# Kernel optimization log

Hardware: AMD Instinct MI355X
Metric: run time of the kernel (lower is better)

Reference implementation:

```python
import jax, jax.numpy as jnp
import numpy as np

B, T = 2, 2048
V, C, H = 32000, 1024, 16
HS = C // H  # 64
W_SCALE = 0.02


def setup_inputs() -> dict:
    key = jax.random.key(0)
    ks = jax.random.split(key, 8)
    x = jax.random.randint(ks[0], (B, T), 0, V)
    tok_emb = jax.random.normal(ks[1], (V, C), jnp.float32) * W_SCALE
    pos_emb = jax.random.normal(ks[2], (T, C), jnp.float32) * W_SCALE
    wq = jax.random.normal(ks[3], (H, C, HS), jnp.float32) * W_SCALE
    wk = jax.random.normal(ks[4], (H, C, HS), jnp.float32) * W_SCALE
    wv = jax.random.normal(ks[5], (H, C, HS), jnp.float32) * W_SCALE
    bq = jnp.zeros((H, HS), jnp.float32)
    bk = jnp.zeros((H, HS), jnp.float32)
    bv = jnp.zeros((H, HS), jnp.float32)
    w_head = jax.random.normal(ks[6], (C, V), jnp.float32) * W_SCALE
    b_head = jnp.zeros((V,), jnp.float32)
    return dict(x=x, tok_emb=tok_emb, pos_emb=pos_emb, wq=wq, bq=bq,
                wk=wk, bk=bk, wv=wv, bv=bv, w_head=w_head, b_head=b_head)


def reference(x, tok_emb, pos_emb, wq, bq, wk, bk, wv, bv, w_head, b_head):
    Bx, Tx = x.shape
    Cx = tok_emb.shape[1]
    h = tok_emb[x] + pos_emb[:Tx]  # [B,T,C]
    # all heads batched: per-head Linear layers stacked on leading H axis
    q = jnp.einsum('btc,hcd->bhtd', h, wq) + bq[None, :, None, :]
    k = jnp.einsum('btc,hcd->bhtd', h, wk) + bk[None, :, None, :]
    v = jnp.einsum('btc,hcd->bhtd', h, wv) + bv[None, :, None, :]
    # NOTE: original scales by n_embd**-0.5 (full C), not head_size**-0.5
    att = jnp.einsum('bhtd,bhsd->bhts', q, k) * (Cx ** -0.5)
    causal = jnp.tril(jnp.ones((Tx, Tx), dtype=bool))
    att = jnp.where(causal, att, jnp.finfo(att.dtype).min)
    att = jax.nn.softmax(att, axis=-1)
    y = jnp.einsum('bhts,bhsd->bhtd', att, v)  # [B,H,T,HS]
    y = jnp.transpose(y, (0, 2, 1, 3)).reshape(Bx, Tx, Cx)  # concat heads
    logits = jnp.einsum('btc,cv->btv', y, w_head) + b_head  # [B,T,V]
    return logits
```

## Files before the change

kernel.cpp:

```cpp
#include <hip/hip_runtime.h>

#define T_SEQ 2048
#define C_DIM 1024
#define H_N   16
#define HS_D  64
#define V_DIM 32000

typedef float f32x4 __attribute__((ext_vector_type(4)));
typedef __bf16 bf16x8 __attribute__((ext_vector_type(8)));
typedef unsigned short us4 __attribute__((ext_vector_type(4)));
typedef unsigned short us8 __attribute__((ext_vector_type(8)));

__device__ inline unsigned short f2bf(float f) {
  unsigned int u = __float_as_uint(f);
  u = (u + 0x7FFFu + ((u >> 16) & 1u)) >> 16;
  return (unsigned short)u;
}

__global__ __launch_bounds__(256) void embed_kernel(
    const int* __restrict__ x, const float* __restrict__ tok,
    const float* __restrict__ pos, unsigned short* __restrict__ h) {
  int idx = blockIdx.x * 256 + threadIdx.x;
  int bt = idx >> 8;
  int c4 = (idx & 255) * 4;
  int t = bt & (T_SEQ - 1);
  int tokid = x[bt];
  f32x4 a = *(const f32x4*)(tok + (size_t)tokid * C_DIM + c4);
  f32x4 b = *(const f32x4*)(pos + (size_t)t * C_DIM + c4);
  f32x4 s = a + b;
  us4 o;
  o[0] = f2bf(s[0]); o[1] = f2bf(s[1]); o[2] = f2bf(s[2]); o[3] = f2bf(s[3]);
  *(us4*)(h + (size_t)bt * C_DIM + c4) = o;
}

__global__ __launch_bounds__(256) void repack_qkv(
    const float* __restrict__ wq, const float* __restrict__ wk, const float* __restrict__ wv,
    const float* __restrict__ bq, const float* __restrict__ bk, const float* __restrict__ bv,
    unsigned short* __restrict__ wt, float* __restrict__ biasp) {
  int which = blockIdx.y;
  const float* w = (which == 0) ? wq : (which == 1) ? wk : wv;
  int i = blockIdx.x * 256 + threadIdx.x;
  int d = i & 63;
  int c = (i >> 6) & (C_DIM - 1);
  int hh = i >> 16;
  int n = which * 1024 + hh * 64 + d;
  wt[(size_t)n * C_DIM + c] = f2bf(w[i]);
  if (c == 0) {
    const float* bb = (which == 0) ? bq : (which == 1) ? bk : bv;
    biasp[n] = bb[hh * 64 + d];
  }
}

__global__ __launch_bounds__(256) void repack_whead(
    const float* __restrict__ wh, unsigned short* __restrict__ wht) {
  __shared__ float tile[64][65];
  int v0 = blockIdx.x * 64;
  int c0 = blockIdx.y * 64;
  int tr = threadIdx.x >> 6;
  int tc = threadIdx.x & 63;
#pragma unroll
  for (int i = 0; i < 16; ++i) {
    int r = i * 4 + tr;
    tile[r][tc] = wh[(size_t)(c0 + r) * V_DIM + v0 + tc];
  }
  __syncthreads();
#pragma unroll
  for (int i = 0; i < 16; ++i) {
    int vr = i * 4 + tr;
    wht[(size_t)(v0 + vr) * C_DIM + c0 + tc] = f2bf(tile[tc][vr]);
  }
}

#define GK 1024
#define GBK 32
#define GNT 32

__global__ __launch_bounds__(512, 2) void gemm256(
    const unsigned short* __restrict__ A, const unsigned short* __restrict__ Bt,
    const float* __restrict__ bias, float* __restrict__ Cout, int N, int Mtiles) {
  __shared__ unsigned short As[4][256 * 32];
  __shared__ unsigned short Bs[4][256 * 32];
  int tid = threadIdx.x;
  int lane = tid & 63;
  int wid = tid >> 6;
  int wm = wid >> 2, wn = wid & 3;
  int l16 = lane & 15, g = lane >> 4;
  int swz = (l16 & 3) ^ ((l16 >> 2) & 3);

  int cpx = gridDim.x >> 3;
  int lin = blockIdx.x;
  int wg = (lin & 7) * cpx + (lin >> 3);
  int m0 = (wg % Mtiles) * 256;
  int n0 = (wg / Mtiles) * 256;

  auto stage = [&](const unsigned short* __restrict__ G, int t0,
                   unsigned short* lds, int kt) {
#pragma unroll
    for (int L = 0; L < 2; ++L) {
      int chunk = L * 512 + tid;
      int row = chunk >> 2;
      int c = (chunk & 3) ^ (row & 3) ^ ((row >> 2) & 3);
      const unsigned short* ga = G + (size_t)(t0 + row) * GK + kt * GBK + c * 8;
      __builtin_amdgcn_global_load_lds(
          (const __attribute__((address_space(1))) void*)ga,
          (__attribute__((address_space(3))) void*)(lds + chunk * 8), 16, 0, 0);
    }
  };

#pragma unroll
  for (int kt = 0; kt < 3; ++kt) {
    stage(A, m0, As[kt], kt);
    stage(Bt, n0, Bs[kt], kt);
  }

  f32x4 acc[8][4] = {};

  for (int t = 0; t < GNT; ++t) {
    int buf = t & 3;
    if (t + 2 < GNT)      asm volatile("s_waitcnt vmcnt(8)" ::: "memory");
    else if (t + 1 < GNT) asm volatile("s_waitcnt vmcnt(4)" ::: "memory");
    else                  asm volatile("s_waitcnt vmcnt(0)" ::: "memory");
    asm volatile("s_barrier" ::: "memory");

    const char* Ab = (const char*)As[buf];
    const char* Bb = (const char*)Bs[buf];

    bf16x8 bfr[4], af[4];
#pragma unroll
    for (int n = 0; n < 4; ++n) {
      int row = wn * 64 + n * 16 + l16;
      bfr[n] = *(const bf16x8*)(Bb + row * 64 + ((g ^ swz) * 16));
    }
#pragma unroll
    for (int m = 0; m < 4; ++m) {
      int row = wm * 128 + m * 16 + l16;
      af[m] = *(const bf16x8*)(Ab + row * 64 + ((g ^ swz) * 16));
    }
    if (t + 3 < GNT) stage(A, m0, As[(t + 3) & 3], t + 3);
    __builtin_amdgcn_s_setprio(1);
#pragma unroll
    for (int m = 0; m < 4; ++m)
#pragma unroll
      for (int n = 0; n < 4; ++n)
        acc[m][n] = __builtin_amdgcn_mfma_f32_16x16x32_bf16(af[m], bfr[n], acc[m][n], 0, 0, 0);
    __builtin_amdgcn_s_setprio(0);
    asm volatile("s_barrier" ::: "memory");

#pragma unroll
    for (int m = 0; m < 4; ++m) {
      int row = wm * 128 + 64 + m * 16 + l16;
      af[m] = *(const bf16x8*)(Ab + row * 64 + ((g ^ swz) * 16));
    }
    if (t + 3 < GNT) stage(Bt, n0, Bs[(t + 3) & 3], t + 3);
    __builtin_amdgcn_s_setprio(1);
#pragma unroll
    for (int m = 0; m < 4; ++m)
#pragma unroll
      for (int n = 0; n < 4; ++n)
        acc[4 + m][n] = __builtin_amdgcn_mfma_f32_16x16x32_bf16(af[m], bfr[n], acc[4 + m][n], 0, 0, 0);
    __builtin_amdgcn_s_setprio(0);
  }

#pragma unroll
  for (int m = 0; m < 8; ++m) {
    int mh = m >> 2, mi = m & 3;
    int row = m0 + wm * 128 + mh * 64 + mi * 16 + g * 4;
#pragma unroll
    for (int n = 0; n < 4; ++n) {
      int col = n0 + wn * 64 + n * 16 + l16;
      float bv = bias[col];
#pragma unroll
      for (int j = 0; j < 4; ++j)
        Cout[(size_t)(row + j) * N + col] = acc[m][n][j] + bv;
    }
  }
}

__global__ __launch_bounds__(256) void attn_mfma(
    const float* __restrict__ qkv, unsigned short* __restrict__ y) {
  __shared__ char lds[24576];
  char* Kl = lds;
  char* Vl = lds + 8192;
  char* Pl = lds + 16384;

  int bh = blockIdx.y;
  int b = bh >> 4, h = bh & 15;
  int qb = (T_SEQ / 64 - 1) - blockIdx.x;
  int tid = threadIdx.x;
  int lane = tid & 63, w = tid >> 6;
  int l16 = lane & 15, g = lane >> 4;
  size_t bT = (size_t)b * T_SEQ;
  const float scale = 0.03125f;

  bf16x8 qf[2];
  {
    const float* qrow = qkv + (bT + qb * 64 + w * 16 + l16) * 3072 + h * 64;
#pragma unroll
    for (int kk = 0; kk < 2; ++kk) {
      f32x4 a = *(const f32x4*)(qrow + kk * 32 + g * 8);
      f32x4 c = *(const f32x4*)(qrow + kk * 32 + g * 8 + 4);
      us8 o;
      o[0] = f2bf(a[0]); o[1] = f2bf(a[1]); o[2] = f2bf(a[2]); o[3] = f2bf(a[3]);
      o[4] = f2bf(c[0]); o[5] = f2bf(c[1]); o[6] = f2bf(c[2]); o[7] = f2bf(c[3]);
      qf[kk] = *(bf16x8*)&o;
    }
  }

  f32x4 yacc[4] = {};
  float mrun[4], lrun[4];
#pragma unroll
  for (int j = 0; j < 4; ++j) { mrun[j] = -3.0e38f; lrun[j] = 0.f; }

  int srow = tid >> 2;
  int c0 = (tid & 3) * 16;

  for (int kb = 0; kb <= qb; ++kb) {
    {
      const float* kp = qkv + (bT + kb * 64 + srow) * 3072 + 1024 + h * 64 + c0;
      f32x4 k0 = *(const f32x4*)(kp + 0);
      f32x4 k1 = *(const f32x4*)(kp + 4);
      f32x4 k2 = *(const f32x4*)(kp + 8);
      f32x4 k3 = *(const f32x4*)(kp + 12);
      us8 pa, pb;
      pa[0]=f2bf(k0[0]); pa[1]=f2bf(k0[1]); pa[2]=f2bf(k0[2]); pa[3]=f2bf(k0[3]);
      pa[4]=f2bf(k1[0]); pa[5]=f2bf(k1[1]); pa[6]=f2bf(k1[2]); pa[7]=f2bf(k1[3]);
      pb[0]=f2bf(k2[0]); pb[1]=f2bf(k2[1]); pb[2]=f2bf(k2[2]); pb[3]=f2bf(k2[3]);
      pb[4]=f2bf(k3[0]); pb[5]=f2bf(k3[1]); pb[6]=f2bf(k3[2]); pb[7]=f2bf(k3[3]);
      *(us8*)(Kl + ((srow * 128 + c0 * 2)      ^ ((srow & 7) << 4))) = pa;
      *(us8*)(Kl + ((srow * 128 + c0 * 2 + 16) ^ ((srow & 7) << 4))) = pb;
      const float* vp = kp + 1024;
      f32x4 v0 = *(const f32x4*)(vp + 0);
      f32x4 v1 = *(const f32x4*)(vp + 4);
      f32x4 v2 = *(const f32x4*)(vp + 8);
      f32x4 v3 = *(const f32x4*)(vp + 12);
      float vals[16] = {v0[0],v0[1],v0[2],v0[3], v1[0],v1[1],v1[2],v1[3],
                        v2[0],v2[1],v2[2],v2[3], v3[0],v3[1],v3[2],v3[3]};
#pragma unroll
      for (int i = 0; i < 16; ++i) {
        int ch = c0 + i;
        *(unsigned short*)(Vl + ((ch * 128 + srow * 2) ^ ((ch & 7) << 4))) = f2bf(vals[i]);
      }
    }
    __syncthreads();

    f32x4 s[4] = {};
#pragma unroll
    for (int kk = 0; kk < 2; ++kk)
#pragma unroll
      for (int n = 0; n < 4; ++n) {
        int krow = n * 16 + l16;
        bf16x8 fb = *(const bf16x8*)(Kl + ((krow * 128 + (kk * 32 + g * 8) * 2) ^ ((krow & 7) << 4)));
        s[n] = __builtin_amdgcn_mfma_f32_16x16x32_bf16(qf[kk], fb, s[n], 0, 0, 0);
      }

    bool diag = (kb == qb);
    float pr[4][4];
    float corr[4];
#pragma unroll
    for (int j = 0; j < 4; ++j) {
      int rloc = w * 16 + g * 4 + j;
      float m = -3.0e38f;
#pragma unroll
      for (int n = 0; n < 4; ++n) {
        float v = s[n][j] * scale;
        if (diag && (n * 16 + l16) > rloc) v = -3.0e38f;
        pr[n][j] = v;
        m = fmaxf(m, v);
      }
      m = fmaxf(m, __shfl_xor(m, 1));
      m = fmaxf(m, __shfl_xor(m, 2));
      m = fmaxf(m, __shfl_xor(m, 4));
      m = fmaxf(m, __shfl_xor(m, 8));
      float mn = fmaxf(mrun[j], m);
      corr[j] = __expf(mrun[j] - mn);
      mrun[j] = mn;
      float ps = 0.f;
#pragma unroll
      for (int n = 0; n < 4; ++n) {
        float e = __expf(pr[n][j] - mn);
        pr[n][j] = e;
        ps += e;
      }
      ps += __shfl_xor(ps, 1);
      ps += __shfl_xor(ps, 2);
      ps += __shfl_xor(ps, 4);
      ps += __shfl_xor(ps, 8);
      lrun[j] = lrun[j] * corr[j] + ps;
    }
#pragma unroll
    for (int n = 0; n < 4; ++n)
#pragma unroll
      for (int j = 0; j < 4; ++j)
        yacc[n][j] *= corr[j];

#pragma unroll
    for (int j = 0; j < 4; ++j) {
      int row = w * 16 + g * 4 + j;
#pragma unroll
      for (int n = 0; n < 4; ++n)
        *(unsigned short*)(Pl + ((row * 128 + (n * 16 + l16) * 2) ^ ((row & 7) << 4))) = f2bf(pr[n][j]);
    }

#pragma unroll
    for (int kk = 0; kk < 2; ++kk) {
      int prow = w * 16 + l16;
      bf16x8 fa = *(const bf16x8*)(Pl + ((prow * 128 + (kk * 32 + g * 8) * 2) ^ ((prow & 7) << 4)));
#pragma unroll
      for (int n = 0; n < 4; ++n) {
        int vrow = n * 16 + l16;
        bf16x8 fb = *(const bf16x8*)(Vl + ((vrow * 128 + (kk * 32 + g * 8) * 2) ^ ((vrow & 7) << 4)));
        yacc[n] = __builtin_amdgcn_mfma_f32_16x16x32_bf16(fa, fb, yacc[n], 0, 0, 0);
      }
    }
    __syncthreads();
  }

#pragma unroll
  for (int j = 0; j < 4; ++j) {
    float inv = 1.0f / lrun[j];
    int row = qb * 64 + w * 16 + g * 4 + j;
    unsigned short* yo = y + (bT + row) * C_DIM + h * 64;
#pragma unroll
    for (int n = 0; n < 4; ++n)
      yo[n * 16 + l16] = f2bf(yacc[n][j] * inv);
  }
}

extern "C" void kernel_launch(void* const* d_in, const int* in_sizes, int n_in,
                              void* d_out, int out_size, void* d_ws, size_t ws_size,
                              hipStream_t stream) {
  const int*   x    = (const int*)d_in[0];
  const float* tok  = (const float*)d_in[1];
  const float* pos  = (const float*)d_in[2];
  const float* wq   = (const float*)d_in[3];
  const float* bq   = (const float*)d_in[4];
  const float* wk   = (const float*)d_in[5];
  const float* bk   = (const float*)d_in[6];
  const float* wv   = (const float*)d_in[7];
  const float* bv   = (const float*)d_in[8];
  const float* wh   = (const float*)d_in[9];
  const float* bhd  = (const float*)d_in[10];
  float* out = (float*)d_out;

  char* ws = (char*)d_ws;
  size_t off = 0;
  auto alloc = [&](size_t bytes) {
    void* p = ws + off;
    off += (bytes + 255) & ~(size_t)255;
    return p;
  };
  unsigned short* h_bf    = (unsigned short*)alloc((size_t)4096 * 1024 * 2);
  unsigned short* wqkv_t  = (unsigned short*)alloc((size_t)3072 * 1024 * 2);
  float*          qbias   = (float*)alloc((size_t)3072 * 4);
  unsigned short* wh_t    = (unsigned short*)alloc((size_t)V_DIM * 1024 * 2);
  float*          qkv     = (float*)alloc((size_t)4096 * 3072 * 4);
  unsigned short* ybf     = (unsigned short*)alloc((size_t)4096 * 1024 * 2);

  embed_kernel<<<4096, 256, 0, stream>>>(x, tok, pos, h_bf);
  repack_qkv<<<dim3(4096, 3), 256, 0, stream>>>(wq, wk, wv, bq, bk, bv, wqkv_t, qbias);
  repack_whead<<<dim3(V_DIM / 64, 16), 256, 0, stream>>>(wh, wh_t);
  gemm256<<<192, 512, 0, stream>>>(h_bf, wqkv_t, qbias, qkv, 3072, 16);
  attn_mfma<<<dim3(T_SEQ / 64, 2 * H_N), 256, 0, stream>>>(qkv, ybf);
  gemm256<<<2000, 512, 0, stream>>>(ybf, wh_t, bhd, out, V_DIM, 16);
}
```

Baseline: 664.9 us.

## Restructure GEMM to single-buffer BK=64 with per-quarter streaming of A tiles

The GEMM drops the 4-deep ring of 32-wide K tiles and uses one 256x64 LDS buffer each for A and B, with an 8-way XOR swizzle. The next A tile is refilled in four row-quarters, each issued right after the matching quarter has been read into registers, while MFMAs on the current data run. B is staged once per K step. This frees LDS so more blocks can be resident and halves the number of K iterations, but adds more barriers and leaves less prefetch depth to hide global latency.

```diff
diff --git a/kernel.cpp b/kernel.cpp
--- a/kernel.cpp
+++ b/kernel.cpp
@@ -72,20 +72,18 @@
 }
 
 #define GK 1024
-#define GBK 32
-#define GNT 32
+#define GNT 16
 
 __global__ __launch_bounds__(512, 2) void gemm256(
     const unsigned short* __restrict__ A, const unsigned short* __restrict__ Bt,
     const float* __restrict__ bias, float* __restrict__ Cout, int N, int Mtiles) {
-  __shared__ unsigned short As[4][256 * 32];
-  __shared__ unsigned short Bs[4][256 * 32];
+  __shared__ unsigned short As[256 * 64];
+  __shared__ unsigned short Bs[256 * 64];
   int tid = threadIdx.x;
   int lane = tid & 63;
   int wid = tid >> 6;
   int wm = wid >> 2, wn = wid & 3;
   int l16 = lane & 15, g = lane >> 4;
-  int swz = (l16 & 3) ^ ((l16 >> 2) & 3);
 
   int cpx = gridDim.x >> 3;
   int lin = blockIdx.x;
@@ -93,85 +91,93 @@
   int m0 = (wg % Mtiles) * 256;
   int n0 = (wg / Mtiles) * 256;
 
-  auto stage = [&](const unsigned short* __restrict__ G, int t0,
-                   unsigned short* lds, int kt) {
-#pragma unroll
-    for (int L = 0; L < 2; ++L) {
-      int chunk = L * 512 + tid;
-      int row = chunk >> 2;
-      int c = (chunk & 3) ^ (row & 3) ^ ((row >> 2) & 3);
-      const unsigned short* ga = G + (size_t)(t0 + row) * GK + kt * GBK + c * 8;
+  auto stageB = [&](int kt) {
+#pragma unroll
+    for (int q = 0; q < 4; ++q) {
+      int chunk = q * 512 + tid;
+      int row = chunk >> 3, cpos = chunk & 7;
+      int c = cpos ^ (row & 7);
+      const unsigned short* src = Bt + (size_t)(n0 + row) * GK + kt * 64 + c * 8;
       __builtin_amdgcn_global_load_lds(
-          (const __attribute__((address_space(1))) void*)ga,
-          (__attribute__((address_space(3))) void*)(lds + chunk * 8), 16, 0, 0);
+          (const __attribute__((address_space(1))) void*)src,
+          (__attribute__((address_space(3))) void*)(Bs + chunk * 8), 16, 0, 0);
     }
   };
-
-#pragma unroll
-  for (int kt = 0; kt < 3; ++kt) {
-    stage(A, m0, As[kt], kt);
-    stage(Bt, n0, Bs[kt], kt);
-  }
+  auto stageA = [&](int kt, int p) {
+    int i = tid;
+    int half = i >> 8;
+    int rowl = (i & 255) >> 3;
+    int row = half * 128 + p * 32 + rowl;
+    int cpos = i & 7;
+    int c = cpos ^ (row & 7);
+    const unsigned short* src = A + (size_t)(m0 + row) * GK + kt * 64 + c * 8;
+    __builtin_amdgcn_global_load_lds(
+        (const __attribute__((address_space(1))) void*)src,
+        (__attribute__((address_space(3))) void*)(As + row * 64 + cpos * 8), 16, 0, 0);
+  };
+
+  stageB(0);
+#pragma unroll
+  for (int p = 0; p < 4; ++p) stageA(0, p);
 
   f32x4 acc[8][4] = {};
 
   for (int t = 0; t < GNT; ++t) {
-    int buf = t & 3;
-    if (t + 2 < GNT)      asm volatile("s_waitcnt vmcnt(8)" ::: "memory");
-    else if (t + 1 < GNT) asm volatile("s_waitcnt vmcnt(4)" ::: "memory");
-    else                  asm volatile("s_waitcnt vmcnt(0)" ::: "memory");
-    asm volatile("s_barrier" ::: "memory");
-
-    const char* Ab = (const char*)As[buf];
-    const char* Bb = (const char*)Bs[buf];
-
-    bf16x8 bfr[4], af[4];
-#pragma unroll
-    for (int n = 0; n < 4; ++n) {
-      int row = wn * 64 + n * 16 + l16;
-      bfr[n] = *(const bf16x8*)(Bb + row * 64 + ((g ^ swz) * 16));
-    }
-#pragma unroll
-    for (int m = 0; m < 4; ++m) {
-      int row = wm * 128 + m * 16 + l16;
-      af[m] = *(const bf16x8*)(Ab + row * 64 + ((g ^ swz) * 16));
-    }
-    if (t + 3 < GNT) stage(A, m0, As[(t + 3) & 3], t + 3);
-    __builtin_amdgcn_s_setprio(1);
-#pragma unroll
-    for (int m = 0; m < 4; ++m)
-#pragma unroll
-      for (int n = 0; n < 4; ++n)
-        acc[m][n] = __builtin_amdgcn_mfma_f32_16x16x32_bf16(af[m], bfr[n], acc[m][n], 0, 0, 0);
-    __builtin_amdgcn_s_setprio(0);
-    asm volatile("s_barrier" ::: "memory");
-
-#pragma unroll
-    for (int m = 0; m < 4; ++m) {
-      int row = wm * 128 + 64 + m * 16 + l16;
-      af[m] = *(const bf16x8*)(Ab + row * 64 + ((g ^ swz) * 16));
-    }
-    if (t + 3 < GNT) stage(Bt, n0, Bs[(t + 3) & 3], t + 3);
-    __builtin_amdgcn_s_setprio(1);
-#pragma unroll
-    for (int m = 0; m < 4; ++m)
-#pragma unroll
-      for (int n = 0; n < 4; ++n)
-        acc[4 + m][n] = __builtin_amdgcn_mfma_f32_16x16x32_bf16(af[m], bfr[n], acc[4 + m][n], 0, 0, 0);
-    __builtin_amdgcn_s_setprio(0);
-  }
-
-#pragma unroll
-  for (int m = 0; m < 8; ++m) {
-    int mh = m >> 2, mi = m & 3;
-    int row = m0 + wm * 128 + mh * 64 + mi * 16 + g * 4;
+    bf16x8 bfr[4][2];
+#pragma unroll
+    for (int p = 0; p < 4; ++p) {
+      if (p == 0) asm volatile("s_waitcnt vmcnt(3)" ::: "memory");
+      else        asm volatile("s_waitcnt vmcnt(7)" ::: "memory");
+      asm volatile("s_barrier" ::: "memory");
+
+      if (p == 0) {
+#pragma unroll
+        for (int n = 0; n < 4; ++n) {
+          int row = wn * 64 + n * 16 + l16;
+#pragma unroll
+          for (int kk = 0; kk < 2; ++kk)
+            bfr[n][kk] = *(const bf16x8*)((const char*)Bs + row * 128 + (((kk * 4 + g) ^ (l16 & 7)) * 16));
+        }
+      }
+      bf16x8 af[2][2];
+#pragma unroll
+      for (int mi = 0; mi < 2; ++mi) {
+        int row = wm * 128 + p * 32 + mi * 16 + l16;
+#pragma unroll
+        for (int kk = 0; kk < 2; ++kk)
+          af[mi][kk] = *(const bf16x8*)((const char*)As + row * 128 + (((kk * 4 + g) ^ (l16 & 7)) * 16));
+      }
+      asm volatile("s_waitcnt lgkmcnt(0)" ::: "memory");
+      asm volatile("s_barrier" ::: "memory");
+
+      if (t + 1 < GNT) {
+        if (p == 0) { stageB(t + 1); stageA(t + 1, 0); }
+        else        stageA(t + 1, p);
+      }
+
+      __builtin_amdgcn_s_setprio(1);
+#pragma unroll
+      for (int mi = 0; mi < 2; ++mi)
+#pragma unroll
+        for (int n = 0; n < 4; ++n)
+#pragma unroll
+          for (int kk = 0; kk < 2; ++kk)
+            acc[2 * p + mi][n] =
+                __builtin_amdgcn_mfma_f32_16x16x32_bf16(af[mi][kk], bfr[n][kk], acc[2 * p + mi][n], 0, 0, 0);
+      __builtin_amdgcn_s_setprio(0);
+    }
+  }
+
+#pragma unroll
+  for (int mf = 0; mf < 8; ++mf) {
+    int row = m0 + wm * 128 + mf * 16 + g * 4;
 #pragma unroll
     for (int n = 0; n < 4; ++n) {
       int col = n0 + wn * 64 + n * 16 + l16;
       float bv = bias[col];
 #pragma unroll
       for (int j = 0; j < 4; ++j)
-        Cout[(size_t)(row + j) * N + col] = acc[m][n][j] + bv;
+        Cout[(size_t)(row + j) * N + col] = acc[mf][n][j] + bv;
     }
   }
 }
```

After: 710.9 us. +6.9%, slower.
